# Kernel tuning notes

Hardware: AMD Instinct MI355X
Metric: run time of the kernel (lower is better)

The kernel has to match this reference:

```python
import jax, jax.numpy as jnp
import numpy as np

N = 10000      # nodes
E = 80000      # directed edges (before self loops)
F_IN = 128     # input feature dim
OUT = 16       # out_channels (classes)


def setup_inputs() -> dict:
    key = jax.random.key(0)
    ks = jax.random.split(key, 20)
    p = lambda k, shape: (jax.random.normal(k, shape, jnp.float32) * 0.1)
    x = jax.random.normal(ks[0], (N, F_IN), jnp.float32)
    edge_index = jax.random.randint(ks[1], (2, E), 0, N, dtype=jnp.int64)
    return {
        "x": x, "edge_index": edge_index,
        # conv1: in=128 -> heads=10, ch=256
        "W1": p(ks[2], (F_IN, 10 * 256)), "as1": p(ks[3], (10, 256)), "ad1": p(ks[4], (10, 256)), "b1": jnp.zeros((10 * 256,), jnp.float32),
        # conv2: in=2560 -> heads=8, ch=56
        "W2": p(ks[5], (2560, 8 * 56)), "as2": p(ks[6], (8, 56)), "ad2": p(ks[7], (8, 56)), "b2": jnp.zeros((8 * 56,), jnp.float32),
        # conv3: in=448 -> heads=4, ch=32
        "W3": p(ks[8], (448, 4 * 32)), "as3": p(ks[9], (4, 32)), "ad3": p(ks[10], (4, 32)), "b3": jnp.zeros((4 * 32,), jnp.float32),
        # conv4: in=128 -> heads=1, ch=OUT, concat=False (mean over heads)
        "W4": p(ks[11], (128, 1 * OUT)), "as4": p(ks[12], (1, OUT)), "ad4": p(ks[13], (1, OUT)), "b4": jnp.zeros((OUT,), jnp.float32),
    }


def _gat_layer(x, src, dst, W, a_src, a_dst, b, heads, ch, concat, n):
    # linear projection -> [n, H, C]
    h = (x @ W).reshape(n, heads, ch)
    # per-node attention halves (PyG decomposition of a^T [h_i || h_j])
    e_src = jnp.einsum('nhc,hc->nh', h, a_src)
    e_dst = jnp.einsum('nhc,hc->nh', h, a_dst)
    # per-edge logits, LeakyReLU(0.2) as in PyG GATConv
    e = jax.nn.leaky_relu(e_src[src] + e_dst[dst], 0.2)  # [E', H]
    # segment softmax over edges grouped by destination node
    m = jax.ops.segment_max(e, dst, num_segments=n)
    m = jnp.where(jnp.isfinite(m), m, 0.0)
    ex = jnp.exp(e - m[dst])
    denom = jax.ops.segment_sum(ex, dst, num_segments=n)
    alpha = ex / (denom[dst] + 1e-16)  # [E', H]
    # weighted scatter-sum of source messages
    out = jax.ops.segment_sum(alpha[:, :, None] * h[src], dst, num_segments=n)  # [n, H, C]
    out = out.reshape(n, heads * ch) if concat else out.mean(axis=1)
    return out + b


def reference(x, edge_index, W1, as1, ad1, b1, W2, as2, ad2, b2,
              W3, as3, ad3, b3, W4, as4, ad4, b4):
    n = x.shape[0]
    loops = jnp.arange(n, dtype=edge_index.dtype)
    src = jnp.concatenate([edge_index[0], loops])  # add_self_loops=True
    dst = jnp.concatenate([edge_index[1], loops])
    lrelu = lambda t: jax.nn.leaky_relu(t, 0.1)  # outer activations in forward()
    h = lrelu(_gat_layer(x, src, dst, W1, as1, ad1, b1, 10, 256, True, n))
    h = lrelu(_gat_layer(h, src, dst, W2, as2, ad2, b2, 8, 56, True, n))
    h = lrelu(_gat_layer(h, src, dst, W3, as3, ad3, b3, 4, 32, True, n))
    h = lrelu(_gat_layer(h, src, dst, W4, as4, ad4, b4, 1, OUT, False, n))
    return jax.nn.softmax(h, axis=1)
```

## Files before the change

kernel.cpp:

```cpp
#include <hip/hip_runtime.h>
#include <math.h>

#define NNODES 10000
#define MPAD   10112
#define NEDGES 80000
#define ETOT   (NEDGES + NNODES)

typedef __attribute__((ext_vector_type(4))) float f32x4;
typedef __attribute__((ext_vector_type(8))) short bf16x8;
typedef __attribute__((ext_vector_type(4))) unsigned int u32x4;

__device__ inline unsigned short f2bf(float f) {
    unsigned int u = __float_as_uint(f);
    unsigned int r = (u + 0x7fffu + ((u >> 16) & 1u)) >> 16;
    return (unsigned short)r;
}
__device__ inline float bf2f(unsigned short h) {
    return __uint_as_float(((unsigned int)h) << 16);
}
__device__ inline float lrelu01(float v) { return (v > 0.f) ? v : 0.1f * v; }
__device__ inline float lrelu02(float v) { return (v > 0.f) ? v : 0.2f * v; }

__global__ void count_deg(const int* __restrict__ ei, int* __restrict__ indeg,
                          int E, int n) {
    int i = blockIdx.x * blockDim.x + threadIdx.x;
    if (i >= E + n) return;
    int dst = (i < E) ? ei[E + i] : (i - E);
    atomicAdd(&indeg[dst], 1);
}

__global__ void scan_rowptr(const int* __restrict__ indeg, int* __restrict__ row_ptr,
                            int* __restrict__ cursor, int n) {
    __shared__ int sums[1024];
    int tid = threadIdx.x;
    int per = (n + 1023) / 1024;
    int start = tid * per;
    int end = start + per; if (end > n) end = n;
    int s = 0;
    for (int i = start; i < end; ++i) s += indeg[i];
    sums[tid] = s;
    __syncthreads();
    for (int off = 1; off < 1024; off <<= 1) {
        int v = (tid >= off) ? sums[tid - off] : 0;
        __syncthreads();
        sums[tid] += v;
        __syncthreads();
    }
    int excl = (tid == 0) ? 0 : sums[tid - 1];
    for (int i = start; i < end; ++i) {
        row_ptr[i] = excl;
        cursor[i]  = excl;
        excl += indeg[i];
    }
    if (tid == 1023) row_ptr[n] = sums[1023];
}

__global__ void scatter_edges(const int* __restrict__ ei, int* __restrict__ cursor,
                              int* __restrict__ col, int E, int n) {
    int i = blockIdx.x * blockDim.x + threadIdx.x;
    if (i >= E + n) return;
    int src, dst;
    if (i < E) { src = ei[i]; dst = ei[E + i]; }
    else       { src = i - E; dst = i - E; }
    int pos = atomicAdd(&cursor[dst], 1);
    col[pos] = src;
}

__global__ void convert_bf16(const float* __restrict__ in, unsigned short* __restrict__ out,
                             int n) {
    int i = blockIdx.x * blockDim.x + threadIdx.x;
    if (i < n) out[i] = f2bf(in[i]);
}

__global__ void transpose_all(const float* __restrict__ W1, const float* __restrict__ W2,
                              const float* __restrict__ W3,
                              unsigned short* __restrict__ W1t,
                              unsigned short* __restrict__ W2t,
                              unsigned short* __restrict__ W3t) {
    __shared__ float t[32][33];
    int b = blockIdx.x;
    const float* W; unsigned short* Wt; int K, N, nb, kb;
    if (b < 320)       { W = W1; Wt = W1t; K = 128;  N = 2560; int i = b;        nb = i % 80; kb = i / 80; }
    else if (b < 1440) { W = W2; Wt = W2t; K = 2560; N = 448;  int i = b - 320;  nb = i % 14; kb = i / 14; }
    else               { W = W3; Wt = W3t; K = 448;  N = 128;  int i = b - 1440; nb = i % 4;  kb = i / 4;  }
    int kb32 = kb * 32, nb32 = nb * 32;
    int tx = threadIdx.x, ty = threadIdx.y;
    #pragma unroll
    for (int i = 0; i < 32; i += 8)
        t[ty + i][tx] = W[(size_t)(kb32 + ty + i) * N + nb32 + tx];
    __syncthreads();
    #pragma unroll
    for (int i = 0; i < 32; i += 8)
        Wt[(size_t)(nb32 + ty + i) * K + kb32 + tx] = f2bf(t[tx][ty + i]);
}

__global__ void make_wsd(const float* __restrict__ W1, const float* __restrict__ as1,
                         const float* __restrict__ ad1,
                         float* __restrict__ wsrc, float* __restrict__ wdst) {
    int idx = blockIdx.x * blockDim.x + threadIdx.x;
    if (idx >= 1280) return;
    int h = idx >> 7, k = idx & 127;
    const float* wrow = W1 + (size_t)k * 2560 + h * 256;
    const float* as = as1 + h * 256;
    const float* ad = ad1 + h * 256;
    float s = 0.f, d = 0.f;
    for (int c = 0; c < 256; c += 4) {
        f32x4 w = *(const f32x4*)&wrow[c];
        f32x4 a = *(const f32x4*)&as[c];
        f32x4 b = *(const f32x4*)&ad[c];
        #pragma unroll
        for (int j = 0; j < 4; ++j) { s += w[j] * a[j]; d += w[j] * b[j]; }
    }
    wsrc[h * 128 + k] = s;
    wdst[h * 128 + k] = d;
}

__global__ __launch_bounds__(256) void e1_dots(const unsigned short* __restrict__ xb,
                                               const float* __restrict__ wsrc,
                                               const float* __restrict__ wdst,
                                               float* __restrict__ e_src,
                                               float* __restrict__ e_dst, int M) {
    __shared__ float ws[1280], wd[1280];
    int tid = threadIdx.x;
    for (int i = tid; i < 1280; i += 256) { ws[i] = wsrc[i]; wd[i] = wdst[i]; }
    __syncthreads();
    int node = blockIdx.x * 4 + (tid >> 6);
    int lane = tid & 63;
    if (node >= M) return;
    unsigned int xv = ((const unsigned int*)xb)[node * 64 + lane];
    float v0 = bf2f((unsigned short)(xv & 0xffffu));
    float v1 = bf2f((unsigned short)(xv >> 16));
    #pragma unroll
    for (int h = 0; h < 10; ++h) {
        float ps = v0 * ws[h * 128 + 2 * lane] + v1 * ws[h * 128 + 2 * lane + 1];
        float pd = v0 * wd[h * 128 + 2 * lane] + v1 * wd[h * 128 + 2 * lane + 1];
        #pragma unroll
        for (int off = 32; off; off >>= 1) {
            ps += __shfl_down(ps, off);
            pd += __shfl_down(pd, off);
        }
        if (lane == 0) { e_src[node * 10 + h] = ps; e_dst[node * 10 + h] = pd; }
    }
}

__global__ __launch_bounds__(64) void agg_x(const unsigned short* __restrict__ xb,
                                            const float* __restrict__ e_src,
                                            const float* __restrict__ e_dst,
                                            const int* __restrict__ row_ptr,
                                            const int* __restrict__ col,
                                            unsigned short* __restrict__ xagg) {
    int node = blockIdx.x;
    int lane = threadIdx.x;
    int rs = row_ptr[node], re = row_ptr[node + 1];
    float edv = (lane < 10) ? e_dst[node * 10 + lane] : 0.f;

    float dn = 0.f;
    float a0[10], a1[10];
    #pragma unroll
    for (int h = 0; h < 10; ++h) { a0[h] = 0.f; a1[h] = 0.f; }
    for (int i = rs; i < re; ++i) {
        int s = col[i];
        float w = 0.f;
        if (lane < 10) w = __expf(lrelu02(e_src[s * 10 + lane] + edv));
        dn += w;
        unsigned int xv = ((const unsigned int*)xb)[s * 64 + lane];
        float v0 = bf2f((unsigned short)(xv & 0xffffu));
        float v1 = bf2f((unsigned short)(xv >> 16));
        #pragma unroll
        for (int h = 0; h < 10; ++h) {
            float wh = __shfl(w, h);
            a0[h] += wh * v0;
            a1[h] += wh * v1;
        }
    }
    #pragma unroll
    for (int h = 0; h < 10; ++h) {
        float rdn = 1.f / (__shfl(dn, h) + 1e-16f);
        unsigned int o = (unsigned int)f2bf(a0[h] * rdn) |
                         ((unsigned int)f2bf(a1[h] * rdn) << 16);
        ((unsigned int*)xagg)[((size_t)node * 10 + h) * 64 + lane] = o;
    }
}

#define GBM 128
#define GBK 32
__global__ __launch_bounds__(256) void gemm_l1(const unsigned short* __restrict__ A,
                                               const unsigned short* __restrict__ Bt,
                                               const float* __restrict__ bias,
                                               unsigned short* __restrict__ C) {
    constexpr int NT = 128, NI = 4, K = 128;
    __shared__ short As[GBM * GBK];
    __shared__ short Bs[NT * GBK];
    int h  = blockIdx.x >> 1;
    int nt = blockIdx.x & 1;
    int bn = h * 256 + nt * 128;
    int bm = blockIdx.y * GBM;
    int tid  = threadIdx.x;
    int wave = tid >> 6, lane = tid & 63;
    int wr = wave >> 1, wc = wave & 1;
    int lrow  = lane >> 2;
    int lkoff = (lane & 3) * 8;
    int row16 = lane & 15;
    int q8    = (lane >> 4) * 8;

    f32x4 acc[4][NI];
    #pragma unroll
    for (int mi = 0; mi < 4; ++mi)
        #pragma unroll
        for (int ni = 0; ni < NI; ++ni) acc[mi][ni] = (f32x4){0.f, 0.f, 0.f, 0.f};

    for (int k0 = 0; k0 < K; k0 += GBK) {
        #pragma unroll
        for (int i = 0; i < 2; ++i) {
            int c = i * 4 + wave;
            int row = c * 16 + lrow;
            const unsigned short* gp = A + ((size_t)(bm + row) * 10 + h) * K + k0 + lkoff;
            __builtin_amdgcn_global_load_lds(
                (const __attribute__((address_space(1))) void*)gp,
                (__attribute__((address_space(3))) void*)&As[c * 512], 16, 0, 0);
        }
        #pragma unroll
        for (int i = 0; i < 2; ++i) {
            int c = i * 4 + wave;
            int row = c * 16 + lrow;
            const unsigned short* gp = Bt + (size_t)(bn + row) * K + k0 + lkoff;
            __builtin_amdgcn_global_load_lds(
                (const __attribute__((address_space(1))) void*)gp,
                (__attribute__((address_space(3))) void*)&Bs[c * 512], 16, 0, 0);
        }
        __syncthreads();
        bf16x8 af[4], bfr[NI];
        #pragma unroll
        for (int mi = 0; mi < 4; ++mi)
            af[mi] = *(const bf16x8*)&As[(wr * 64 + mi * 16 + row16) * GBK + q8];
        #pragma unroll
        for (int ni = 0; ni < NI; ++ni)
            bfr[ni] = *(const bf16x8*)&Bs[(wc * 64 + ni * 16 + row16) * GBK + q8];
        #pragma unroll
        for (int mi = 0; mi < 4; ++mi)
            #pragma unroll
            for (int ni = 0; ni < NI; ++ni)
                acc[mi][ni] = __builtin_amdgcn_mfma_f32_16x16x32_bf16(
                    af[mi], bfr[ni], acc[mi][ni], 0, 0, 0);
        __syncthreads();
    }

    int rbase = bm + wr * 64 + (lane >> 4) * 4;
    #pragma unroll
    for (int mi = 0; mi < 4; ++mi)
        #pragma unroll
        for (int ni = 0; ni < NI; ++ni) {
            int cc = bn + wc * 64 + ni * 16 + (lane & 15);
            float b = bias[cc];
            #pragma unroll
            for (int r = 0; r < 4; ++r) {
                float v = lrelu01(acc[mi][ni][r] + b);
                C[(size_t)(rbase + mi * 16 + r) * 2560 + cc] = f2bf(v);
            }
        }
}

template <int NT, bool SWIZ>
__global__ __launch_bounds__(256) void gemm_mfma(const unsigned short* __restrict__ A,
                                                 const unsigned short* __restrict__ Bt,
                                                 unsigned short* __restrict__ C,
                                                 int N, int nbn, int K, int klen) {
    constexpr int NI = NT / 32;
    __shared__ short As[GBM * GBK];
    __shared__ short Bs[NT * GBK];
    int bn, bm, kbeg, kend;
    size_t zoff = 0;
    if constexpr (SWIZ) {
        int b = blockIdx.x;
        int x = b & 7, t = b >> 3;
        int j = x + 8 * (t / nbn);
        if (j >= MPAD / GBM) return;
        bn = (t % nbn) * NT;
        bm = j * GBM;
        kbeg = blockIdx.y * klen;
        kend = kbeg + klen;
        zoff = (size_t)blockIdx.y * MPAD * N;
    } else {
        bn = blockIdx.x * NT;
        bm = blockIdx.y * GBM;
        kbeg = 0; kend = K;
    }
    int tid  = threadIdx.x;
    int wave = tid >> 6, lane = tid & 63;
    int wr = wave >> 1, wc = wave & 1;
    int lrow  = lane >> 2;
    int lkoff = (lane & 3) * 8;
    int row16 = lane & 15;
    int q8    = (lane >> 4) * 8;

    f32x4 acc[4][NI];
    #pragma unroll
    for (int mi = 0; mi < 4; ++mi)
        #pragma unroll
        for (int ni = 0; ni < NI; ++ni) acc[mi][ni] = (f32x4){0.f, 0.f, 0.f, 0.f};

    for (int k0 = kbeg; k0 < kend; k0 += GBK) {
        #pragma unroll
        for (int i = 0; i < 2; ++i) {
            int c = i * 4 + wave;
            int row = c * 16 + lrow;
            const unsigned short* gp = A + (size_t)(bm + row) * K + k0 + lkoff;
            __builtin_amdgcn_global_load_lds(
                (const __attribute__((address_space(1))) void*)gp,
                (__attribute__((address_space(3))) void*)&As[c * 512], 16, 0, 0);
        }
        #pragma unroll
        for (int i = 0; i < NT / 64; ++i) {
            int c = i * 4 + wave;
            int row = c * 16 + lrow;
            const unsigned short* gp = Bt + (size_t)(bn + row) * K + k0 + lkoff;
            __builtin_amdgcn_global_load_lds(
                (const __attribute__((address_space(1))) void*)gp,
                (__attribute__((address_space(3))) void*)&Bs[c * 512], 16, 0, 0);
        }
        __syncthreads();
        bf16x8 af[4], bfr[NI];
        #pragma unroll
        for (int mi = 0; mi < 4; ++mi)
            af[mi] = *(const bf16x8*)&As[(wr * 64 + mi * 16 + row16) * GBK + q8];
        #pragma unroll
        for (int ni = 0; ni < NI; ++ni)
            bfr[ni] = *(const bf16x8*)&Bs[(wc * (NT / 2) + ni * 16 + row16) * GBK + q8];
        #pragma unroll
        for (int mi = 0; mi < 4; ++mi)
            #pragma unroll
            for (int ni = 0; ni < NI; ++ni)
                acc[mi][ni] = __builtin_amdgcn_mfma_f32_16x16x32_bf16(
                    af[mi], bfr[ni], acc[mi][ni], 0, 0, 0);
        __syncthreads();
    }

    int rbase = bm + wr * 64 + (lane >> 4) * 4;
    int cbase = bn + wc * (NT / 2) + (lane & 15);
    #pragma unroll
    for (int mi = 0; mi < 4; ++mi)
        #pragma unroll
        for (int ni = 0; ni < NI; ++ni)
            #pragma unroll
            for (int r = 0; r < 4; ++r)
                C[zoff + (size_t)(rbase + mi * 16 + r) * N + cbase + ni * 16] =
                    f2bf(acc[mi][ni][r]);
}

__global__ void reduce2p(const unsigned int* __restrict__ P, unsigned int* __restrict__ out,
                         int n2) {
    int i = blockIdx.x * blockDim.x + threadIdx.x;
    if (i >= n2) return;
    unsigned int a = P[i];
    unsigned int b = P[(size_t)MPAD * 448 / 2 + i];
    float lo = bf2f((unsigned short)(a & 0xffffu)) + bf2f((unsigned short)(b & 0xffffu));
    float hi = bf2f((unsigned short)(a >> 16))     + bf2f((unsigned short)(b >> 16));
    out[i] = (unsigned int)f2bf(lo) | ((unsigned int)f2bf(hi) << 16);
}

__global__ __launch_bounds__(256) void gemm4_attn(const unsigned short* __restrict__ A,
                                                  const float* __restrict__ W,
                                                  const float* __restrict__ as4,
                                                  const float* __restrict__ ad4,
                                                  unsigned short* __restrict__ C,
                                                  float* __restrict__ e_src,
                                                  float* __restrict__ e_dst, int M) {
    __shared__ float Ws[128 * 16];
    int tid = threadIdx.x;
    for (int i = tid; i < 2048; i += 256) Ws[i] = W[i];
    __syncthreads();
    int node = blockIdx.x * 16 + (tid >> 4);
    int n = tid & 15;
    if (node >= M) return;
    const unsigned short* ap = A + (size_t)node * 128;
    float acc = 0.f;
    #pragma unroll 8
    for (int k = 0; k < 128; ++k)
        acc += bf2f(ap[k]) * Ws[k * 16 + n];
    C[(size_t)node * 16 + n] = f2bf(acc);
    float vs = acc * as4[n];
    float vd = acc * ad4[n];
    #pragma unroll
    for (int off = 1; off < 16; off <<= 1) {
        vs += __shfl_xor(vs, off);
        vd += __shfl_xor(vd, off);
    }
    if (n == 0) { e_src[node] = vs; e_dst[node] = vd; }
}

template <int H, int C>
__global__ __launch_bounds__(64) void attn_small(const unsigned short* __restrict__ h,
                                                 const float* __restrict__ a_src,
                                                 const float* __restrict__ a_dst,
                                                 float* __restrict__ e_src,
                                                 float* __restrict__ e_dst) {
    constexpr int LPH = 64 / H;
    constexpr int CPL = C / LPH;
    int node = blockIdx.x;
    int lane = threadIdx.x;
    int head = lane / LPH;
    int k = lane - head * LPH;
    const unsigned short* hp = h + (size_t)node * (H * C) + head * C + k * CPL;
    const float* as = a_src + head * C + k * CPL;
    const float* ad = a_dst + head * C + k * CPL;
    float s1 = 0.f, s2 = 0.f;
    #pragma unroll
    for (int c = 0; c < CPL; ++c) {
        float v = bf2f(hp[c]);
        s1 += v * as[c];
        s2 += v * ad[c];
    }
    #pragma unroll
    for (int off = LPH / 2; off; off >>= 1) {
        s1 += __shfl_down(s1, off);
        s2 += __shfl_down(s2, off);
    }
    if (k == 0) { e_src[node * H + head] = s1; e_dst[node * H + head] = s2; }
}

__global__ __launch_bounds__(64) void agg_l2(const unsigned short* __restrict__ h,
                                             const float* __restrict__ e_src,
                                             const float* __restrict__ e_dst,
                                             const int* __restrict__ row_ptr,
                                             const int* __restrict__ col,
                                             const float* __restrict__ bias,
                                             unsigned short* __restrict__ out) {
    const int H = 8;
    int node = blockIdx.x;
    int lane = threadIdx.x;
    bool act = lane < 56;
    int head = act ? (lane / 7) : 0;
    int cpos = act ? (lane - head * 7) : 0;
    int rs = row_ptr[node], re = row_ptr[node + 1];
    float edv = e_dst[node * H + head];

    float dn = 0.f;
    float acc0[8], acc1[8];
    #pragma unroll
    for (int k = 0; k < 8; ++k) { acc0[k] = 0.f; acc1[k] = 0.f; }
    int i = rs;
    for (; i + 1 < re; i += 2) {
        int s0 = col[i], s1 = col[i + 1];
        float es0 = e_src[s0 * H + head];
        float es1 = e_src[s1 * H + head];
        u32x4 hv0 = *(const u32x4*)(h + (size_t)s0 * 448 + head * 56 + cpos * 8);
        u32x4 hv1 = *(const u32x4*)(h + (size_t)s1 * 448 + head * 56 + cpos * 8);
        float w0 = __expf(lrelu02(es0 + edv));
        float w1 = __expf(lrelu02(es1 + edv));
        dn += w0 + w1;
        #pragma unroll
        for (int d = 0; d < 4; ++d) {
            acc0[2 * d]     += w0 * bf2f((unsigned short)(hv0[d] & 0xffffu));
            acc0[2 * d + 1] += w0 * bf2f((unsigned short)(hv0[d] >> 16));
            acc1[2 * d]     += w1 * bf2f((unsigned short)(hv1[d] & 0xffffu));
            acc1[2 * d + 1] += w1 * bf2f((unsigned short)(hv1[d] >> 16));
        }
    }
    if (i < re) {
        int s = col[i];
        float w = __expf(lrelu02(e_src[s * H + head] + edv));
        dn += w;
        u32x4 hv = *(const u32x4*)(h + (size_t)s * 448 + head * 56 + cpos * 8);
        #pragma unroll
        for (int d = 0; d < 4; ++d) {
            acc0[2 * d]     += w * bf2f((unsigned short)(hv[d] & 0xffffu));
            acc0[2 * d + 1] += w * bf2f((unsigned short)(hv[d] >> 16));
        }
    }
    float rdn = 1.f / (dn + 1e-16f);

    if (act) {
        const float* bp = bias + head * 56 + cpos * 8;
        u32x4 o;
        #pragma unroll
        for (int d = 0; d < 4; ++d) {
            float v0 = lrelu01((acc0[2 * d] + acc1[2 * d]) * rdn + bp[2 * d]);
            float v1 = lrelu01((acc0[2 * d + 1] + acc1[2 * d + 1]) * rdn + bp[2 * d + 1]);
            o[d] = (unsigned int)f2bf(v0) | ((unsigned int)f2bf(v1) << 16);
        }
        *(u32x4*)(out + (size_t)node * 448 + head * 56 + cpos * 8) = o;
    }
}

__global__ __launch_bounds__(64) void agg_l3(const unsigned short* __restrict__ h,
                                             const float* __restrict__ e_src,
                                             const float* __restrict__ e_dst,
                                             const int* __restrict__ row_ptr,
                                             const int* __restrict__ col,
                                             const float* __restrict__ bias,
                                             unsigned short* __restrict__ out) {
    const int H = 4;
    int node = blockIdx.x;
    int lane = threadIdx.x;
    bool act = lane < 16;
    int head = (lane >> 2) & 3;
    int cpos = lane & 3;
    int rs = row_ptr[node], re = row_ptr[node + 1];
    float edv = e_dst[node * H + head];

    float dn = 0.f;
    float acc0[8], acc1[8];
    #pragma unroll
    for (int k = 0; k < 8; ++k) { acc0[k] = 0.f; acc1[k] = 0.f; }
    int i = rs;
    for (; i + 1 < re; i += 2) {
        int s0 = col[i], s1 = col[i + 1];
        float es0 = e_src[s0 * H + head];
        float es1 = e_src[s1 * H + head];
        u32x4 hv0 = *(const u32x4*)(h + (size_t)s0 * 128 + head * 32 + cpos * 8);
        u32x4 hv1 = *(const u32x4*)(h + (size_t)s1 * 128 + head * 32 + cpos * 8);
        float w0 = __expf(lrelu02(es0 + edv));
        float w1 = __expf(lrelu02(es1 + edv));
        dn += w0 + w1;
        #pragma unroll
        for (int d = 0; d < 4; ++d) {
            acc0[2 * d]     += w0 * bf2f((unsigned short)(hv0[d] & 0xffffu));
            acc0[2 * d + 1] += w0 * bf2f((unsigned short)(hv0[d] >> 16));
            acc1[2 * d]     += w1 * bf2f((unsigned short)(hv1[d] & 0xffffu));
            acc1[2 * d + 1] += w1 * bf2f((unsigned short)(hv1[d] >> 16));
        }
    }
    if (i < re) {
        int s = col[i];
        float w = __expf(lrelu02(e_src[s * H + head] + edv));
        dn += w;
        u32x4 hv = *(const u32x4*)(h + (size_t)s * 128 + head * 32 + cpos * 8);
        #pragma unroll
        for (int d = 0; d < 4; ++d) {
            acc0[2 * d]     += w * bf2f((unsigned short)(hv[d] & 0xffffu));
            acc0[2 * d + 1] += w * bf2f((unsigned short)(hv[d] >> 16));
        }
    }
    float rdn = 1.f / (dn + 1e-16f);

    if (act) {
        const float* bp = bias + head * 32 + cpos * 8;
        u32x4 o;
        #pragma unroll
        for (int d = 0; d < 4; ++d) {
            float v0 = lrelu01((acc0[2 * d] + acc1[2 * d]) * rdn + bp[2 * d]);
            float v1 = lrelu01((acc0[2 * d + 1] + acc1[2 * d + 1]) * rdn + bp[2 * d + 1]);
            o[d] = (unsigned int)f2bf(v0) | ((unsigned int)f2bf(v1) << 16);
        }
        *(u32x4*)(out + (size_t)node * 128 + head * 32 + cpos * 8) = o;
    }
}

__global__ __launch_bounds__(64) void agg4_softmax(const unsigned int* __restrict__ h2,
                                                   const float* __restrict__ e_src,
                                                   const float* __restrict__ e_dst,
                                                   const int* __restrict__ row_ptr,
                                                   const int* __restrict__ col,
                                                   const float* __restrict__ bias,
                                                   float* __restrict__ out) {
    int node = blockIdx.x;
    int lane = threadIdx.x;
    int cpos = lane & 7;
    int rs = row_ptr[node], re = row_ptr[node + 1];
    float edv = e_dst[node];

    float dn = 0.f, a0 = 0.f, a1 = 0.f;
    for (int i = rs; i < re; ++i) {
        int s = col[i];
        float w = __expf(lrelu02(e_src[s] + edv));
        dn += w;
        unsigned int hv = h2[(size_t)s * 8 + cpos];
        a0 += w * bf2f((unsigned short)(hv & 0xffffu));
        a1 += w * bf2f((unsigned short)(hv >> 16));
    }
    float rdn = 1.f / (dn + 1e-16f);
    float v0 = lrelu01(a0 * rdn + bias[2 * cpos]);
    float v1 = lrelu01(a1 * rdn + bias[2 * cpos + 1]);

    float m = fmaxf(v0, v1);
    #pragma unroll
    for (int off = 4; off; off >>= 1) m = fmaxf(m, __shfl_xor(m, off));
    float e0 = __expf(v0 - m), e1 = __expf(v1 - m);
    float s = e0 + e1;
    #pragma unroll
    for (int off = 4; off; off >>= 1) s += __shfl_xor(s, off);
    float r = 1.f / s;
    if (lane < 8) {
        out[node * 16 + 2 * cpos]     = e0 * r;
        out[node * 16 + 2 * cpos + 1] = e1 * r;
    }
}

extern "C" void kernel_launch(void* const* d_in, const int* in_sizes, int n_in,
                              void* d_out, int out_size, void* d_ws, size_t ws_size,
                              hipStream_t stream) {
    const float* x   = (const float*)d_in[0];
    const int*   ei  = (const int*)d_in[1];
    const float* W1  = (const float*)d_in[2];
    const float* as1 = (const float*)d_in[3];
    const float* ad1 = (const float*)d_in[4];
    const float* b1  = (const float*)d_in[5];
    const float* W2  = (const float*)d_in[6];
    const float* as2 = (const float*)d_in[7];
    const float* ad2 = (const float*)d_in[8];
    const float* b2  = (const float*)d_in[9];
    const float* W3  = (const float*)d_in[10];
    const float* as3 = (const float*)d_in[11];
    const float* ad3 = (const float*)d_in[12];
    const float* b3  = (const float*)d_in[13];
    const float* W4  = (const float*)d_in[14];
    const float* as4 = (const float*)d_in[15];
    const float* ad4 = (const float*)d_in[16];
    const float* b4  = (const float*)d_in[17];

    char* ws = (char*)d_ws;
    size_t off = 0;
    auto alloc = [&](size_t bytes) -> void* {
        void* p = ws + off;
        off = (off + bytes + 255) & ~(size_t)255;
        return p;
    };
    unsigned short* hbuf = (unsigned short*)alloc((size_t)MPAD * 2560 * sizeof(short));
    unsigned short* abuf = (unsigned short*)alloc((size_t)MPAD * 2560 * sizeof(short));
    unsigned short* pbuf = (unsigned short*)alloc((size_t)2 * MPAD * 448 * sizeof(short));
    unsigned short* xagg = (unsigned short*)alloc((size_t)MPAD * 10 * 128 * sizeof(short));
    unsigned short* W1t  = (unsigned short*)alloc((size_t)2560 * 128 * sizeof(short));
    unsigned short* W2t  = (unsigned short*)alloc((size_t)448 * 2560 * sizeof(short));
    unsigned short* W3t  = (unsigned short*)alloc((size_t)128 * 448 * sizeof(short));
    float* wsrc   = (float*)alloc((size_t)10 * 128 * sizeof(float));
    float* wdst   = (float*)alloc((size_t)10 * 128 * sizeof(float));
    float* e_src  = (float*)alloc((size_t)NNODES * 10 * sizeof(float));
    float* e_dst  = (float*)alloc((size_t)NNODES * 10 * sizeof(float));
    int* indeg    = (int*)alloc(NNODES * sizeof(int));
    int* row_ptr  = (int*)alloc((NNODES + 1) * sizeof(int));
    int* cursor   = (int*)alloc(NNODES * sizeof(int));
    int* col      = (int*)alloc(ETOT * sizeof(int));
    (void)ws_size;

    hipMemsetAsync(indeg, 0, NNODES * sizeof(int), stream);
    int eb = (ETOT + 255) / 256;
    count_deg<<<eb, 256, 0, stream>>>(ei, indeg, NEDGES, NNODES);
    scan_rowptr<<<1, 1024, 0, stream>>>(indeg, row_ptr, cursor, NNODES);
    scatter_edges<<<eb, 256, 0, stream>>>(ei, cursor, col, NEDGES, NNODES);

    transpose_all<<<1496, dim3(32, 8), 0, stream>>>(W1, W2, W3, W1t, W2t, W3t);
    make_wsd<<<20, 64, 0, stream>>>(W1, as1, ad1, wsrc, wdst);
    convert_bf16<<<(NNODES * 128 + 255) / 256, 256, 0, stream>>>(x, abuf, NNODES * 128);

    const int Mb = MPAD / GBM;

    e1_dots<<<(NNODES + 3) / 4, 256, 0, stream>>>(abuf, wsrc, wdst, e_src, e_dst, NNODES);
    agg_x<<<NNODES, 64, 0, stream>>>(abuf, e_src, e_dst, row_ptr, col, xagg);
    gemm_l1<<<dim3(20, Mb), 256, 0, stream>>>(xagg, W1t, b1, abuf);

    gemm_mfma<64, true><<<dim3(8 * 7 * 10, 2), 256, 0, stream>>>(
        abuf, W2t, pbuf, 448, 7, 2560, 1280);
    {
        int n2 = NNODES * 448 / 2;
        reduce2p<<<(n2 + 255) / 256, 256, 0, stream>>>(
            (const unsigned int*)pbuf, (unsigned int*)hbuf, n2);
    }
    attn_small<8, 56><<<NNODES, 64, 0, stream>>>(hbuf, as2, ad2, e_src, e_dst);
    agg_l2<<<NNODES, 64, 0, stream>>>(hbuf, e_src, e_dst, row_ptr, col, b2, abuf);

    gemm_mfma<64, false><<<dim3(2, Mb), 256, 0, stream>>>(
        abuf, W3t, hbuf, 128, 1, 448, 448);
    attn_small<4, 32><<<NNODES, 64, 0, stream>>>(hbuf, as3, ad3, e_src, e_dst);
    agg_l3<<<NNODES, 64, 0, stream>>>(hbuf, e_src, e_dst, row_ptr, col, b3, abuf);

    gemm4_attn<<<(NNODES + 15) / 16, 256, 0, stream>>>(
        abuf, W4, as4, ad4, hbuf, e_src, e_dst, NNODES);
    agg4_softmax<<<NNODES, 64, 0, stream>>>(
        (const unsigned int*)hbuf, e_src, e_dst, row_ptr, col, b4, (float*)d_out);
}
```

Baseline: 301.4 us.

## Swizzle GEMM LDS tiles and deepen split-K for layers two and three

Applies an XOR swizzle to the k-chunk offset in both the global-to-LDS loads and the MFMA fragment reads of the bf16 GEMMs, to reduce LDS bank conflicts. Layer 2's GEMM goes from 2-way to 4-way split-K, and layer 3's GEMM gains a 2-way split-K, both reduced by a new templated reduction kernel. The aim is more workgroups on the device for these short, skinny GEMMs. The cost is extra partial-sum traffic through a larger workspace, one more kernel launch, and an extra bf16 rounding of each partial.

```diff
diff --git a/kernel.cpp b/kernel.cpp
--- a/kernel.cpp
+++ b/kernel.cpp
@@ -181,6 +181,7 @@
         ((unsigned int*)xagg)[((size_t)node * 10 + h) * 64 + lane] = o;
     }
 }
+
 
 #define GBM 128
 #define GBK 32
@@ -199,9 +200,9 @@
     int wave = tid >> 6, lane = tid & 63;
     int wr = wave >> 1, wc = wave & 1;
     int lrow  = lane >> 2;
-    int lkoff = (lane & 3) * 8;
+    int lk    = (((lane & 3) ^ ((lrow >> 1) & 3))) * 8;
     int row16 = lane & 15;
-    int q8    = (lane >> 4) * 8;
+    int qs    = (((lane >> 4) ^ ((row16 >> 1) & 3))) * 8;
 
     f32x4 acc[4][NI];
     #pragma unroll
@@ -214,7 +215,7 @@
         for (int i = 0; i < 2; ++i) {
             int c = i * 4 + wave;
             int row = c * 16 + lrow;
-            const unsigned short* gp = A + ((size_t)(bm + row) * 10 + h) * K + k0 + lkoff;
+            const unsigned short* gp = A + ((size_t)(bm + row) * 10 + h) * K + k0 + lk;
             __builtin_amdgcn_global_load_lds(
                 (const __attribute__((address_space(1))) void*)gp,
                 (__attribute__((address_space(3))) void*)&As[c * 512], 16, 0, 0);
@@ -223,7 +224,7 @@
         for (int i = 0; i < 2; ++i) {
             int c = i * 4 + wave;
             int row = c * 16 + lrow;
-            const unsigned short* gp = Bt + (size_t)(bn + row) * K + k0 + lkoff;
+            const unsigned short* gp = Bt + (size_t)(bn + row) * K + k0 + lk;
             __builtin_amdgcn_global_load_lds(
                 (const __attribute__((address_space(1))) void*)gp,
                 (__attribute__((address_space(3))) void*)&Bs[c * 512], 16, 0, 0);
@@ -232,10 +233,10 @@
         bf16x8 af[4], bfr[NI];
         #pragma unroll
         for (int mi = 0; mi < 4; ++mi)
-            af[mi] = *(const bf16x8*)&As[(wr * 64 + mi * 16 + row16) * GBK + q8];
+            af[mi] = *(const bf16x8*)&As[(wr * 64 + mi * 16 + row16) * GBK + qs];
         #pragma unroll
         for (int ni = 0; ni < NI; ++ni)
-            bfr[ni] = *(const bf16x8*)&Bs[(wc * 64 + ni * 16 + row16) * GBK + q8];
+            bfr[ni] = *(const bf16x8*)&Bs[(wc * 64 + ni * 16 + row16) * GBK + qs];
         #pragma unroll
         for (int mi = 0; mi < 4; ++mi)
             #pragma unroll
@@ -289,9 +290,9 @@
     int wave = tid >> 6, lane = tid & 63;
     int wr = wave >> 1, wc = wave & 1;
     int lrow  = lane >> 2;
-    int lkoff = (lane & 3) * 8;
+    int lk    = (((lane & 3) ^ ((lrow >> 1) & 3))) * 8;
     int row16 = lane & 15;
-    int q8    = (lane >> 4) * 8;
+    int qs    = (((lane >> 4) ^ ((row16 >> 1) & 3))) * 8;
 
     f32x4 acc[4][NI];
     #pragma unroll
@@ -304,7 +305,7 @@
         for (int i = 0; i < 2; ++i) {
             int c = i * 4 + wave;
             int row = c * 16 + lrow;
-            const unsigned short* gp = A + (size_t)(bm + row) * K + k0 + lkoff;
+            const unsigned short* gp = A + (size_t)(bm + row) * K + k0 + lk;
             __builtin_amdgcn_global_load_lds(
                 (const __attribute__((address_space(1))) void*)gp,
                 (__attribute__((address_space(3))) void*)&As[c * 512], 16, 0, 0);
@@ -313,7 +314,7 @@
         for (int i = 0; i < NT / 64; ++i) {
             int c = i * 4 + wave;
             int row = c * 16 + lrow;
-            const unsigned short* gp = Bt + (size_t)(bn + row) * K + k0 + lkoff;
+            const unsigned short* gp = Bt + (size_t)(bn + row) * K + k0 + lk;
             __builtin_amdgcn_global_load_lds(
                 (const __attribute__((address_space(1))) void*)gp,
                 (__attribute__((address_space(3))) void*)&Bs[c * 512], 16, 0, 0);
@@ -322,10 +323,10 @@
         bf16x8 af[4], bfr[NI];
         #pragma unroll
         for (int mi = 0; mi < 4; ++mi)
-            af[mi] = *(const bf16x8*)&As[(wr * 64 + mi * 16 + row16) * GBK + q8];
+            af[mi] = *(const bf16x8*)&As[(wr * 64 + mi * 16 + row16) * GBK + qs];
         #pragma unroll
         for (int ni = 0; ni < NI; ++ni)
-            bfr[ni] = *(const bf16x8*)&Bs[(wc * (NT / 2) + ni * 16 + row16) * GBK + q8];
+            bfr[ni] = *(const bf16x8*)&Bs[(wc * (NT / 2) + ni * 16 + row16) * GBK + qs];
         #pragma unroll
         for (int mi = 0; mi < 4; ++mi)
             #pragma unroll
@@ -347,14 +348,18 @@
                     f2bf(acc[mi][ni][r]);
 }
 
-__global__ void reduce2p(const unsigned int* __restrict__ P, unsigned int* __restrict__ out,
-                         int n2) {
+template <int S>
+__global__ void reduce_k(const unsigned int* __restrict__ P, unsigned int* __restrict__ out,
+                         size_t stride, int n2) {
     int i = blockIdx.x * blockDim.x + threadIdx.x;
     if (i >= n2) return;
-    unsigned int a = P[i];
-    unsigned int b = P[(size_t)MPAD * 448 / 2 + i];
-    float lo = bf2f((unsigned short)(a & 0xffffu)) + bf2f((unsigned short)(b & 0xffffu));
-    float hi = bf2f((unsigned short)(a >> 16))     + bf2f((unsigned short)(b >> 16));
+    float lo = 0.f, hi = 0.f;
+    #pragma unroll
+    for (int s = 0; s < S; ++s) {
+        unsigned int v = P[s * stride + i];
+        lo += bf2f((unsigned short)(v & 0xffffu));
+        hi += bf2f((unsigned short)(v >> 16));
+    }
     out[i] = (unsigned int)f2bf(lo) | ((unsigned int)f2bf(hi) << 16);
 }
 
@@ -617,7 +622,7 @@
     };
     unsigned short* hbuf = (unsigned short*)alloc((size_t)MPAD * 2560 * sizeof(short));
     unsigned short* abuf = (unsigned short*)alloc((size_t)MPAD * 2560 * sizeof(short));
-    unsigned short* pbuf = (unsigned short*)alloc((size_t)2 * MPAD * 448 * sizeof(short));
+    unsigned short* pbuf = (unsigned short*)alloc((size_t)4 * MPAD * 448 * sizeof(short));
     unsigned short* xagg = (unsigned short*)alloc((size_t)MPAD * 10 * 128 * sizeof(short));
     unsigned short* W1t  = (unsigned short*)alloc((size_t)2560 * 128 * sizeof(short));
     unsigned short* W2t  = (unsigned short*)alloc((size_t)448 * 2560 * sizeof(short));
@@ -648,18 +653,23 @@
     agg_x<<<NNODES, 64, 0, stream>>>(abuf, e_src, e_dst, row_ptr, col, xagg);
     gemm_l1<<<dim3(20, Mb), 256, 0, stream>>>(xagg, W1t, b1, abuf);
 
-    gemm_mfma<64, true><<<dim3(8 * 7 * 10, 2), 256, 0, stream>>>(
-        abuf, W2t, pbuf, 448, 7, 2560, 1280);
+    gemm_mfma<64, true><<<dim3(8 * 7 * 10, 4), 256, 0, stream>>>(
+        abuf, W2t, pbuf, 448, 7, 2560, 640);
     {
         int n2 = NNODES * 448 / 2;
-        reduce2p<<<(n2 + 255) / 256, 256, 0, stream>>>(
-            (const unsigned int*)pbuf, (unsigned int*)hbuf, n2);
+        reduce_k<4><<<(n2 + 255) / 256, 256, 0, stream>>>(
+            (const unsigned int*)pbuf, (unsigned int*)hbuf, (size_t)MPAD * 448 / 2, n2);
     }
     attn_small<8, 56><<<NNODES, 64, 0, stream>>>(hbuf, as2, ad2, e_src, e_dst);
     agg_l2<<<NNODES, 64, 0, stream>>>(hbuf, e_src, e_dst, row_ptr, col, b2, abuf);
 
-    gemm_mfma<64, false><<<dim3(2, Mb), 256, 0, stream>>>(
-        abuf, W3t, hbuf, 128, 1, 448, 448);
+    gemm_mfma<64, true><<<dim3(8 * 2 * 10, 2), 256, 0, stream>>>(
+        abuf, W3t, pbuf, 128, 2, 448, 224);
+    {
+        int n2 = NNODES * 128 / 2;
+        reduce_k<2><<<(n2 + 255) / 256, 256, 0, stream>>>(
+            (const unsigned int*)pbuf, (unsigned int*)hbuf, (size_t)MPAD * 128 / 2, n2);
+    }
     attn_small<4, 32><<<NNODES, 64, 0, stream>>>(hbuf, as3, ad3, e_src, e_dst);
     agg_l3<<<NNODES, 64, 0, stream>>>(hbuf, e_src, e_dst, row_ptr, col, b3, abuf);
 
```

New measurement: 299.8 us. Within noise of the previous version (-0.5%).
